# Performance work log

Hardware: AMD Instinct MI355X
Metric: run time of the kernel (lower is better)

## Reference

```python
import jax, jax.numpy as jnp
import numpy as np

IN_DIM = 128
OUT_DIM = 128
NUM_HEADS = 8
HEAD_DIM = OUT_DIM // NUM_HEADS  # 16
FFN_DIM = OUT_DIM * 2
LN_EPS = 1e-5


def _layer_norm(x, g, b):
    mu = jnp.mean(x, axis=-1, keepdims=True)
    var = jnp.var(x, axis=-1, keepdims=True)
    return (x - mu) * jax.lax.rsqrt(var + LN_EPS) * g + b


def setup_inputs() -> dict:
    key = jax.random.key(0)
    ks = jax.random.split(key, 12)
    B, N = 4, 2048
    s_in = 1.0 / np.sqrt(IN_DIM)
    s_out = 1.0 / np.sqrt(OUT_DIM)
    s_ffn = 1.0 / np.sqrt(FFN_DIM)
    return {
        "adj_matrix": jax.random.randint(ks[0], (N, N), 0, 2, dtype=jnp.int32),
        "h": jax.random.normal(ks[1], (B, N, IN_DIM), dtype=jnp.float32),
        # Q/K/V: Linear(in_dim, out_dim) with use_bias=False, stored as [in, out]
        "Wq": jax.random.uniform(ks[2], (IN_DIM, OUT_DIM), jnp.float32, -s_in, s_in),
        "Wk": jax.random.uniform(ks[3], (IN_DIM, OUT_DIM), jnp.float32, -s_in, s_in),
        "Wv": jax.random.uniform(ks[4], (IN_DIM, OUT_DIM), jnp.float32, -s_in, s_in),
        "Wo": jax.random.uniform(ks[5], (OUT_DIM, OUT_DIM), jnp.float32, -s_out, s_out),
        "bo": jnp.zeros((OUT_DIM,), jnp.float32),
        "ln1_g": jnp.ones((OUT_DIM,), jnp.float32),
        "ln1_b": jnp.zeros((OUT_DIM,), jnp.float32),
        "W1": jax.random.uniform(ks[6], (OUT_DIM, FFN_DIM), jnp.float32, -s_out, s_out),
        "b1": jnp.zeros((FFN_DIM,), jnp.float32),
        "W2": jax.random.uniform(ks[7], (FFN_DIM, OUT_DIM), jnp.float32, -s_ffn, s_ffn),
        "b2": jnp.zeros((OUT_DIM,), jnp.float32),
        "ln2_g": jnp.ones((OUT_DIM,), jnp.float32),
        "ln2_b": jnp.zeros((OUT_DIM,), jnp.float32),
    }


def reference(adj_matrix, h, Wq, Wk, Wv, Wo, bo, ln1_g, ln1_b,
              W1, b1, W2, b2, ln2_g, ln2_b):
    B, N, _ = h.shape
    # QKV projections -> [B, N, H, D]
    Q = (h @ Wq).reshape(B, N, NUM_HEADS, HEAD_DIM)
    K = (h @ Wk).reshape(B, N, NUM_HEADS, HEAD_DIM)
    V = (h @ Wv).reshape(B, N, NUM_HEADS, HEAD_DIM)
    scores = jnp.einsum('bnhd,bmhd->bhnm', Q, K) / jnp.sqrt(
        jnp.asarray(HEAD_DIM, jnp.float32))
    # adjacency-masked attention: mask broadcast over batch and heads
    mask = (adj_matrix == 0)[None, None, :, :]  # [1,1,N,N]
    scores = jnp.where(mask, -jnp.inf, scores)
    attn = jax.nn.softmax(scores, axis=-1)
    attn_out = jnp.einsum('bhnm,bmhd->bnhd', attn, V).reshape(B, N, OUT_DIM)
    # output projection + residual + LN
    x = h + (attn_out @ Wo + bo)
    x = _layer_norm(x, ln1_g, ln1_b)
    # FFN + residual + LN
    y = jax.nn.relu(x @ W1 + b1) @ W2 + b2
    x = _layer_norm(x + y, ln2_g, ln2_b)
    return x
```

## Files before the change

kernel.cpp:

```cpp
#include <hip/hip_runtime.h>

#define B_   4
#define N_   2048
#define DIM  128
#define NH   8
#define HD   16
#define FFN_ 256
#define LN_EPS 1e-5f
#define BN   (B_*N_)
#define LOG2E 1.44269504f

#if __has_builtin(__builtin_amdgcn_exp2f)
#define EXP2(x) __builtin_amdgcn_exp2f(x)
#else
#define EXP2(x) exp2f(x)
#endif

#if __has_builtin(__builtin_amdgcn_sbfe)
#define SBFE1(w, p) ((unsigned)__builtin_amdgcn_sbfe((int)(w), (p), 1))
#else
#define SBFE1(w, p) ((unsigned)(((int)((w) << (31 - (p)))) >> 31))
#endif

typedef __bf16 bf16x8 __attribute__((ext_vector_type(8)));
typedef short  s16x8  __attribute__((ext_vector_type(8)));
typedef float  f32x16 __attribute__((ext_vector_type(16)));
typedef unsigned int u32x4 __attribute__((ext_vector_type(4)));

template<class T> struct as_short_vec { using type = s16x8; };

template <class T>
__device__ auto mfma_try(T a, T b, f32x16 c, int)
    -> decltype(__builtin_amdgcn_mfma_f32_32x32x16_bf16(a, b, c, 0, 0, 0)) {
  return __builtin_amdgcn_mfma_f32_32x32x16_bf16(a, b, c, 0, 0, 0);
}
template <class T>
__device__ f32x16 mfma_try(T a, T b, f32x16 c, long) {
  return __builtin_amdgcn_mfma_f32_32x32x16_bf16(
      __builtin_bit_cast(typename as_short_vec<T>::type, a),
      __builtin_bit_cast(typename as_short_vec<T>::type, b), c, 0, 0, 0);
}
__device__ __forceinline__ f32x16 mfma_bf(bf16x8 a, bf16x8 b, f32x16 c) {
  return mfma_try(a, b, c, 0);
}

__global__ __launch_bounds__(256) void k_prep(
    const int* __restrict__ adj, const float* __restrict__ h,
    const float* __restrict__ W1, const float* __restrict__ W2,
    const float* __restrict__ Wq, const float* __restrict__ Wk,
    const float* __restrict__ Wv, const float* __restrict__ Wo,
    unsigned int* __restrict__ adjbT, __bf16* __restrict__ hb,
    __bf16* __restrict__ W1t, __bf16* __restrict__ W2t,
    __bf16* __restrict__ Wqt, __bf16* __restrict__ Wkt,
    __bf16* __restrict__ Wvt, __bf16* __restrict__ Wot) {
    const int blk = blockIdx.x;
    const int tid = threadIdx.x;
    if (blk < 16384) {
        long long idx = (long long)blk * 256 + tid;
        int v = adj[idx] != 0;
        unsigned long long m = __ballot(v);
        if ((tid & 63) == 0) {
            int q  = (int)(idx >> 11);
            int kc = ((int)idx & 2047) >> 5;
            adjbT[(size_t)kc * 2048 + q]       = (unsigned)m;
            adjbT[(size_t)(kc + 1) * 2048 + q] = (unsigned)(m >> 32);
        }
    } else if (blk < 16896) {
        const int g = (blk - 16384) * 256 + tid;
        const float* src = h + (size_t)g * 8;
        float4 f0 = *(const float4*)src, f1 = *(const float4*)(src + 4);
        bf16x8 v;
        v[0] = (__bf16)f0.x; v[1] = (__bf16)f0.y; v[2] = (__bf16)f0.z; v[3] = (__bf16)f0.w;
        v[4] = (__bf16)f1.x; v[5] = (__bf16)f1.y; v[6] = (__bf16)f1.z; v[7] = (__bf16)f1.w;
        *(bf16x8*)(hb + (size_t)g * 8) = v;
    } else {
        const int g = (blk - 16896) * 256 + tid;
        {
            int k = g >> 8, n = g & 255;
            W1t[(size_t)n * 128 + k] = (__bf16)W1[(size_t)k * 256 + n];
        }
        {
            int k = g >> 7, n = g & 127;
            W2t[(size_t)n * 256 + k] = (__bf16)W2[(size_t)k * 128 + n];
        }
        if (g < 16384) {
            int k = g >> 7, n = g & 127;
            size_t s = (size_t)k * 128 + n, d = (size_t)n * 128 + k;
            Wqt[d] = (__bf16)(Wq[s] * (0.25f * LOG2E));
            Wkt[d] = (__bf16)Wk[s];
            Wvt[d] = (__bf16)Wv[s];
            Wot[d] = (__bf16)Wo[s];
        }
    }
}

__global__ __launch_bounds__(256) void k_qkv(
    const __bf16* __restrict__ hb,
    const __bf16* __restrict__ Wqt, const __bf16* __restrict__ Wkt,
    const __bf16* __restrict__ Wvt,
    __bf16* __restrict__ Qb, __bf16* __restrict__ Kb, __bf16* __restrict__ Vt) {
    const int r0   = blockIdx.x * 32;
    const int tid  = threadIdx.x;
    const int w    = tid >> 6;
    const int lane = tid & 63;
    const int l31  = lane & 31, hi = lane >> 5;

    __shared__ __bf16 Hs[32 * 128];

    for (int i = tid; i < 512; i += 256) {
        int row = i >> 4, u = i & 15;
        bf16x8 v = *(const bf16x8*)(hb + (size_t)(r0 + row) * DIM + u * 8);
        int byte = (row * 256 + u * 16) ^ ((row & 7) << 4);
        *(bf16x8*)((char*)Hs + byte) = v;
    }
    __syncthreads();

    f32x16 aq, ak, av;
    #pragma unroll
    for (int i = 0; i < 16; ++i) { aq[i] = 0.f; ak[i] = 0.f; av[i] = 0.f; }
    #pragma unroll
    for (int kk = 0; kk < 8; ++kk) {
        int byte = (l31 * 256 + kk * 32 + hi * 16) ^ ((l31 & 7) << 4);
        bf16x8 a = *(const bf16x8*)((const char*)Hs + byte);
        const size_t wo = (size_t)(w * 32 + l31) * 128 + kk * 16 + hi * 8;
        aq = mfma_bf(a, *(const bf16x8*)(Wqt + wo), aq);
        ak = mfma_bf(a, *(const bf16x8*)(Wkt + wo), ak);
        av = mfma_bf(a, *(const bf16x8*)(Wvt + wo), av);
    }
    const int n  = w * 32 + l31;
    const int hh = n >> 4, d = n & 15;
    const int b  = r0 >> 11;
    const size_t qbase = (size_t)(b * NH + hh) * N_;
    const size_t vbase = ((size_t)(b * NH + hh) * HD + d) * N_;
    #pragma unroll
    for (int r = 0; r < 16; ++r) {
        int mm   = (r & 3) + 8 * (r >> 2) + 4 * hi;
        int nloc = (r0 & (N_ - 1)) + mm;
        size_t qk = (qbase + nloc) * HD + d;
        Qb[qk] = (__bf16)aq[r];
        Kb[qk] = (__bf16)ak[r];
        int gg = (nloc >> 2) & 7;
        int ng = (gg & 4) | ((gg & 1) << 1) | ((gg >> 1) & 1);
        Vt[vbase + ((nloc & ~31) | (ng << 2) | (nloc & 3))] = (__bf16)av[r];
    }
}

__global__ __launch_bounds__(512, 4) void k_attn(
    const __bf16* __restrict__ Qb, const __bf16* __restrict__ Kb,
    const __bf16* __restrict__ Vt, const unsigned int* __restrict__ adjbT,
    __bf16* __restrict__ AOb) {
    const int bid  = (blockIdx.x & 7) * 256 + (blockIdx.x >> 3);
    const int qt   = bid & 63;
    const int hh   = (bid >> 6) & 7;
    const int b    = bid >> 9;
    const int kq   = threadIdx.x >> 6;
    const int lane = threadIdx.x & 63;
    const int l31  = lane & 31, hi = lane >> 5;
    const int q     = qt * 32 + l31;
    const int kbase = kq * 256;
    const int NT    = 8;

    __shared__ float accL[7][64][9];

    const __bf16* Qh = Qb + (size_t)(b * NH + hh) * N_ * HD;
    const __bf16* Kh = Kb + (size_t)(b * NH + hh) * N_ * HD;
    const __bf16* Vh = Vt + ((size_t)(b * NH + hh) * HD + (l31 & 15)) * N_;
    const unsigned int* wp = adjbT + (size_t)(kq * NT) * 2048 + q;
    const bool vload = (l31 < 16);
    const bf16x8 ones8 = __builtin_bit_cast(bf16x8,
        u32x4{0x3F803F80u, 0x3F803F80u, 0x3F803F80u, 0x3F803F80u});

    bf16x8 qf = *(const bf16x8*)(Qh + (size_t)q * HD + hi * 8);

    f32x16 acc;
    #pragma unroll
    for (int i = 0; i < 16; ++i) acc[i] = 0.f;
    const f32x16 z = {};

    bf16x8 kf  = *(const bf16x8*)(Kh + (size_t)(kbase + l31) * HD + hi * 8);
    bf16x8 vfa = vload ? *(const bf16x8*)(Vh + kbase + hi * 8)      : ones8;
    bf16x8 vfb = vload ? *(const bf16x8*)(Vh + kbase + 16 + hi * 8) : ones8;
    unsigned int w32 = wp[0];

    for (int t = 0; t < NT; ++t) {
        const int tn = (t + 1 < NT) ? t + 1 : t;
        const int k1 = kbase + tn * 32;
        bf16x8 kf_n = *(const bf16x8*)(Kh + (size_t)(k1 + l31) * HD + hi * 8);
        bf16x8 vfa_n = vload ? *(const bf16x8*)(Vh + k1 + hi * 8)      : ones8;
        bf16x8 vfb_n = vload ? *(const bf16x8*)(Vh + k1 + 16 + hi * 8) : ones8;
        unsigned int w32_n = wp[(size_t)tn * 2048];

        f32x16 st = mfma_bf(kf, qf, z);

        float p[16];
        #pragma unroll
        for (int r = 0; r < 16; ++r) p[r] = EXP2(st[r]);
        bf16x8 pa, pb;
        #pragma unroll
        for (int r = 0; r < 8; ++r) { pa[r] = (__bf16)p[r]; pb[r] = (__bf16)p[r + 8]; }

        {
            const unsigned ws = w32 >> (4 * hi);
            u32x4 mA, mB;
            #pragma unroll
            for (int j = 0; j < 4; ++j) {
                const int pj = ((2 * j) & 3) + 8 * ((2 * j) >> 2);
                mA[j] = (SBFE1(ws, pj)      & 0xFFFFu) | (SBFE1(ws, pj + 1)  & 0xFFFF0000u);
                mB[j] = (SBFE1(ws, pj + 16) & 0xFFFFu) | (SBFE1(ws, pj + 17) & 0xFFFF0000u);
            }
            pa = __builtin_bit_cast(bf16x8, __builtin_bit_cast(u32x4, pa) & mA);
            pb = __builtin_bit_cast(bf16x8, __builtin_bit_cast(u32x4, pb) & mB);
        }

        acc = mfma_bf(vfa, pa, acc);
        acc = mfma_bf(vfb, pb, acc);

        kf = kf_n; vfa = vfa_n; vfb = vfb_n; w32 = w32_n;
    }

    if (kq != 0) {
        #pragma unroll
        for (int r = 0; r < 9; ++r) accL[kq - 1][lane][r] = acc[r];
    }
    __syncthreads();
    if (kq == 0) {
        float tot[9];
        #pragma unroll
        for (int r = 0; r < 9; ++r) {
            float v = acc[r];
            #pragma unroll
            for (int i = 0; i < 7; ++i) v += accL[i][lane][r];
            tot[r] = v;
        }
        float inv = 1.f / tot[8];
        bf16x8 ov;
        #pragma unroll
        for (int r = 0; r < 8; ++r) ov[r] = (__bf16)(tot[r] * inv);
        u32x4 ou = __builtin_bit_cast(u32x4, ov);
        __bf16* op = AOb + ((size_t)(b * N_ + q)) * DIM + hh * HD + 4 * hi;
        uint2 w0 = { ou[0], ou[1] }, w1 = { ou[2], ou[3] };
        *(uint2*)op       = w0;
        *(uint2*)(op + 8) = w1;
    }
}

__global__ __launch_bounds__(256) void k_proj_ln(
    const __bf16* __restrict__ AOb, const float* __restrict__ h,
    const __bf16* __restrict__ Wot, const float* __restrict__ bo,
    const float* __restrict__ g, const float* __restrict__ bln,
    __bf16* __restrict__ Xb) {
    const int r0   = blockIdx.x * 32;
    const int tid  = threadIdx.x;
    const int w    = tid >> 6;
    const int lane = tid & 63;
    const int l31  = lane & 31, hi = lane >> 5;

    __shared__ __bf16 As[32 * 128];
    __shared__ float  vv[32][DIM];

    for (int i = tid; i < 512; i += 256) {
        int row = i >> 4, u = i & 15;
        bf16x8 v = *(const bf16x8*)(AOb + (size_t)(r0 + row) * DIM + u * 8);
        int byte = (row * 256 + u * 16) ^ ((row & 7) << 4);
        *(bf16x8*)((char*)As + byte) = v;
    }
    __syncthreads();

    f32x16 acc;
    #pragma unroll
    for (int i = 0; i < 16; ++i) acc[i] = 0.f;
    #pragma unroll
    for (int kk = 0; kk < 8; ++kk) {
        int byte = (l31 * 256 + kk * 32 + hi * 16) ^ ((l31 & 7) << 4);
        bf16x8 a = *(const bf16x8*)((const char*)As + byte);
        acc = mfma_bf(a, *(const bf16x8*)(Wot + (size_t)(w * 32 + l31) * 128 + kk * 16 + hi * 8), acc);
    }
    {
        int n = w * 32 + l31;
        float bb = bo[n];
        #pragma unroll
        for (int r = 0; r < 16; ++r) {
            int mm = (r & 3) + 8 * (r >> 2) + 4 * hi;
            vv[mm][n] = acc[r] + bb + h[(size_t)(r0 + mm) * DIM + n];
        }
    }
    __syncthreads();

    const int ln = lane;
    float gc0 = g[ln], bc0 = bln[ln], gc1 = g[ln + 64], bc1 = bln[ln + 64];
    #pragma unroll
    for (int i = 0; i < 8; ++i) {
        int rr = w * 8 + i;
        float x0 = vv[rr][ln], x1 = vv[rr][ln + 64];
        float s = x0 + x1, s2 = x0 * x0 + x1 * x1;
        for (int off = 1; off < 64; off <<= 1) {
            s  += __shfl_xor(s,  off);
            s2 += __shfl_xor(s2, off);
        }
        float mu  = s * (1.f / DIM);
        float var = s2 * (1.f / DIM) - mu * mu;
        float rs  = rsqrtf(var + LN_EPS);
        size_t o = (size_t)(r0 + rr) * DIM;
        Xb[o + ln]      = (__bf16)((x0 - mu) * rs * gc0 + bc0);
        Xb[o + ln + 64] = (__bf16)((x1 - mu) * rs * gc1 + bc1);
    }
}

__global__ __launch_bounds__(256) void k_ffn_ln(
    const __bf16* __restrict__ Xb,
    const __bf16* __restrict__ W1t, const float* __restrict__ b1,
    const __bf16* __restrict__ W2t, const float* __restrict__ b2,
    const float* __restrict__ g, const float* __restrict__ bln,
    float* __restrict__ out) {
    const int r0   = blockIdx.x * 32;
    const int tid  = threadIdx.x;
    const int w    = tid >> 6;
    const int lane = tid & 63;
    const int l31  = lane & 31, hi = lane >> 5;

    __shared__ __bf16 Xs[32 * 128];
    __shared__ __bf16 Ts[32 * 256];
    __shared__ float  vv[32][DIM];

    for (int i = tid; i < 512; i += 256) {
        int row = i >> 4, u = i & 15;
        bf16x8 v = *(const bf16x8*)(Xb + (size_t)(r0 + row) * DIM + u * 8);
        int byte = (row * 256 + u * 16) ^ ((row & 7) << 4);
        *(bf16x8*)((char*)Xs + byte) = v;
    }
    __syncthreads();

    f32x16 acc1a, acc1b;
    #pragma unroll
    for (int i = 0; i < 16; ++i) { acc1a[i] = 0.f; acc1b[i] = 0.f; }
    #pragma unroll
    for (int kk = 0; kk < 8; ++kk) {
        int byte = (l31 * 256 + kk * 32 + hi * 16) ^ ((l31 & 7) << 4);
        bf16x8 a = *(const bf16x8*)((const char*)Xs + byte);
        bf16x8 bA = *(const bf16x8*)(W1t + (size_t)(w * 32 + l31) * 128 + kk * 16 + hi * 8);
        bf16x8 bB = *(const bf16x8*)(W1t + (size_t)((w + 4) * 32 + l31) * 128 + kk * 16 + hi * 8);
        acc1a = mfma_bf(a, bA, acc1a);
        acc1b = mfma_bf(a, bB, acc1b);
    }
    #pragma unroll
    for (int ct = 0; ct < 2; ++ct) {
        const f32x16& ac = ct ? acc1b : acc1a;
        int n = (w + ct * 4) * 32 + l31;
        float bb = b1[n];
        #pragma unroll
        for (int r = 0; r < 16; ++r) {
            int mm = (r & 3) + 8 * (r >> 2) + 4 * hi;
            float v = fmaxf(ac[r] + bb, 0.f);
            int byte = (mm * 512 + n * 2) ^ ((mm & 7) << 4);
            *(__bf16*)((char*)Ts + byte) = (__bf16)v;
        }
    }
    __syncthreads();

    f32x16 acc2;
    #pragma unroll
    for (int i = 0; i < 16; ++i) acc2[i] = 0.f;
    #pragma unroll
    for (int kk = 0; kk < 16; ++kk) {
        int byte = (l31 * 512 + kk * 32 + hi * 16) ^ ((l31 & 7) << 4);
        bf16x8 a = *(const bf16x8*)((const char*)Ts + byte);
        bf16x8 bb = *(const bf16x8*)(W2t + (size_t)(w * 32 + l31) * 256 + kk * 16 + hi * 8);
        acc2 = mfma_bf(a, bb, acc2);
    }
    {
        int n = w * 32 + l31;
        float bb = b2[n];
        #pragma unroll
        for (int r = 0; r < 16; ++r) {
            int mm = (r & 3) + 8 * (r >> 2) + 4 * hi;
            int byteR = (mm * 256 + n * 2) ^ ((mm & 7) << 4);
            float resid = (float)*(const __bf16*)((const char*)Xs + byteR);
            vv[mm][n] = acc2[r] + bb + resid;
        }
    }
    __syncthreads();

    const int ln = lane;
    float gc0 = g[ln], bc0 = bln[ln], gc1 = g[ln + 64], bc1 = bln[ln + 64];
    #pragma unroll
    for (int i = 0; i < 8; ++i) {
        int rr = w * 8 + i;
        float x0 = vv[rr][ln], x1 = vv[rr][ln + 64];
        float s = x0 + x1, s2 = x0 * x0 + x1 * x1;
        for (int off = 1; off < 64; off <<= 1) {
            s  += __shfl_xor(s,  off);
            s2 += __shfl_xor(s2, off);
        }
        float mu  = s * (1.f / DIM);
        float var = s2 * (1.f / DIM) - mu * mu;
        float rs  = rsqrtf(var + LN_EPS);
        size_t o = (size_t)(r0 + rr) * DIM;
        out[o + ln]      = (x0 - mu) * rs * gc0 + bc0;
        out[o + ln + 64] = (x1 - mu) * rs * gc1 + bc1;
    }
}

extern "C" void kernel_launch(void* const* d_in, const int* in_sizes, int n_in,
                              void* d_out, int out_size, void* d_ws, size_t ws_size,
                              hipStream_t stream) {
    const int*   adj = (const int*)  d_in[0];
    const float* h   = (const float*)d_in[1];
    const float* Wq  = (const float*)d_in[2];
    const float* Wk  = (const float*)d_in[3];
    const float* Wv  = (const float*)d_in[4];
    const float* Wo  = (const float*)d_in[5];
    const float* bo  = (const float*)d_in[6];
    const float* g1  = (const float*)d_in[7];
    const float* b1l = (const float*)d_in[8];
    const float* W1  = (const float*)d_in[9];
    const float* b1  = (const float*)d_in[10];
    const float* W2  = (const float*)d_in[11];
    const float* b2  = (const float*)d_in[12];
    const float* g2  = (const float*)d_in[13];
    const float* b2l = (const float*)d_in[14];
    float* out = (float*)d_out;

    __bf16* AOb = (__bf16*)d_ws;
    unsigned int* adjbT = (unsigned int*)(AOb + (size_t)BN * DIM);
    __bf16* Qb  = (__bf16*)(adjbT + (size_t)64 * 2048);
    __bf16* Kb  = Qb + (size_t)BN * DIM;
    __bf16* Vt  = Kb + (size_t)BN * DIM;
    __bf16* Xb  = Vt + (size_t)BN * DIM;
    __bf16* hb  = Xb + (size_t)BN * DIM;
    __bf16* W1t = hb + (size_t)BN * DIM;
    __bf16* W2t = W1t + (size_t)DIM * FFN_;
    __bf16* Wqt = W2t + (size_t)DIM * FFN_;
    __bf16* Wkt = Wqt + (size_t)DIM * DIM;
    __bf16* Wvt = Wkt + (size_t)DIM * DIM;
    __bf16* Wot = Wvt + (size_t)DIM * DIM;

    hipLaunchKernelGGL(k_prep, dim3(16384 + 512 + 128), dim3(256), 0, stream,
                       adj, h, W1, W2, Wq, Wk, Wv, Wo,
                       adjbT, hb, W1t, W2t, Wqt, Wkt, Wvt, Wot);
    hipLaunchKernelGGL(k_qkv, dim3(BN / 32), dim3(256), 0, stream,
                       hb, Wqt, Wkt, Wvt, Qb, Kb, Vt);
    hipLaunchKernelGGL(k_attn, dim3(B_ * NH * (N_ / 32)), dim3(512), 0, stream,
                       Qb, Kb, Vt, adjbT, AOb);
    hipLaunchKernelGGL(k_proj_ln, dim3(BN / 32), dim3(256), 0, stream,
                       AOb, h, Wot, bo, g1, b1l, Xb);
    hipLaunchKernelGGL(k_ffn_ln, dim3(BN / 32), dim3(256), 0, stream,
                       Xb, W1t, b1, W2t, b2, g2, b2l, out);
}
```

Measured before the change: 65.82 us.

## Fuse h conversion into QKV, merge proj/FFN kernels, use LUT for mask expansion

Converts h from float to bf16 directly inside the QKV kernel instead of a separate prep pass, removing the hb buffer round trip. Merges the output-projection+LN1 kernel with the FFN+LN2 kernel so the normalized activations stay in shared memory rather than going through global Xb, saving one launch. In attention, replaces per-bit sign-extract mask construction with a 16-entry shared-memory lookup table of uint2 masks. The fused tail kernel uses more shared memory per block, which may lower occupancy.

```diff
diff --git a/kernel.cpp b/kernel.cpp
--- a/kernel.cpp
+++ b/kernel.cpp
@@ -16,12 +16,6 @@
 #define EXP2(x) exp2f(x)
 #endif
 
-#if __has_builtin(__builtin_amdgcn_sbfe)
-#define SBFE1(w, p) ((unsigned)__builtin_amdgcn_sbfe((int)(w), (p), 1))
-#else
-#define SBFE1(w, p) ((unsigned)(((int)((w) << (31 - (p)))) >> 31))
-#endif
-
 typedef __bf16 bf16x8 __attribute__((ext_vector_type(8)));
 typedef short  s16x8  __attribute__((ext_vector_type(8)));
 typedef float  f32x16 __attribute__((ext_vector_type(16)));
@@ -45,11 +39,11 @@
 }
 
 __global__ __launch_bounds__(256) void k_prep(
-    const int* __restrict__ adj, const float* __restrict__ h,
+    const int* __restrict__ adj,
     const float* __restrict__ W1, const float* __restrict__ W2,
     const float* __restrict__ Wq, const float* __restrict__ Wk,
     const float* __restrict__ Wv, const float* __restrict__ Wo,
-    unsigned int* __restrict__ adjbT, __bf16* __restrict__ hb,
+    unsigned int* __restrict__ adjbT,
     __bf16* __restrict__ W1t, __bf16* __restrict__ W2t,
     __bf16* __restrict__ Wqt, __bf16* __restrict__ Wkt,
     __bf16* __restrict__ Wvt, __bf16* __restrict__ Wot) {
@@ -65,16 +59,8 @@
             adjbT[(size_t)kc * 2048 + q]       = (unsigned)m;
             adjbT[(size_t)(kc + 1) * 2048 + q] = (unsigned)(m >> 32);
         }
-    } else if (blk < 16896) {
+    } else {
         const int g = (blk - 16384) * 256 + tid;
-        const float* src = h + (size_t)g * 8;
-        float4 f0 = *(const float4*)src, f1 = *(const float4*)(src + 4);
-        bf16x8 v;
-        v[0] = (__bf16)f0.x; v[1] = (__bf16)f0.y; v[2] = (__bf16)f0.z; v[3] = (__bf16)f0.w;
-        v[4] = (__bf16)f1.x; v[5] = (__bf16)f1.y; v[6] = (__bf16)f1.z; v[7] = (__bf16)f1.w;
-        *(bf16x8*)(hb + (size_t)g * 8) = v;
-    } else {
-        const int g = (blk - 16896) * 256 + tid;
         {
             int k = g >> 8, n = g & 255;
             W1t[(size_t)n * 128 + k] = (__bf16)W1[(size_t)k * 256 + n];
@@ -95,7 +81,7 @@
 }
 
 __global__ __launch_bounds__(256) void k_qkv(
-    const __bf16* __restrict__ hb,
+    const float* __restrict__ h,
     const __bf16* __restrict__ Wqt, const __bf16* __restrict__ Wkt,
     const __bf16* __restrict__ Wvt,
     __bf16* __restrict__ Qb, __bf16* __restrict__ Kb, __bf16* __restrict__ Vt) {
@@ -109,7 +95,11 @@
 
     for (int i = tid; i < 512; i += 256) {
         int row = i >> 4, u = i & 15;
-        bf16x8 v = *(const bf16x8*)(hb + (size_t)(r0 + row) * DIM + u * 8);
+        const float* src = h + (size_t)(r0 + row) * DIM + u * 8;
+        float4 f0 = *(const float4*)src, f1 = *(const float4*)(src + 4);
+        bf16x8 v;
+        v[0] = (__bf16)f0.x; v[1] = (__bf16)f0.y; v[2] = (__bf16)f0.z; v[3] = (__bf16)f0.w;
+        v[4] = (__bf16)f1.x; v[5] = (__bf16)f1.y; v[6] = (__bf16)f1.z; v[7] = (__bf16)f1.w;
         int byte = (row * 256 + u * 16) ^ ((row & 7) << 4);
         *(bf16x8*)((char*)Hs + byte) = v;
     }
@@ -161,6 +151,14 @@
     const int NT    = 8;
 
     __shared__ float accL[7][64][9];
+    __shared__ uint2 lutM[16];
+
+    if (threadIdx.x < 16) {
+        unsigned v = threadIdx.x;
+        lutM[v].x = ((v & 1u) ? 0xFFFFu : 0u) | ((v & 2u) ? 0xFFFF0000u : 0u);
+        lutM[v].y = ((v & 4u) ? 0xFFFFu : 0u) | ((v & 8u) ? 0xFFFF0000u : 0u);
+    }
+    __syncthreads();
 
     const __bf16* Qh = Qb + (size_t)(b * NH + hh) * N_ * HD;
     const __bf16* Kh = Kb + (size_t)(b * NH + hh) * N_ * HD;
@@ -183,6 +181,12 @@
     unsigned int w32 = wp[0];
 
     for (int t = 0; t < NT; ++t) {
+        const unsigned ws = w32 >> (4 * hi);
+        uint2 e0 = lutM[ws & 15u];
+        uint2 e1 = lutM[(ws >> 8) & 15u];
+        uint2 e2 = lutM[(ws >> 16) & 15u];
+        uint2 e3 = lutM[(ws >> 24) & 15u];
+
         const int tn = (t + 1 < NT) ? t + 1 : t;
         const int k1 = kbase + tn * 32;
         bf16x8 kf_n = *(const bf16x8*)(Kh + (size_t)(k1 + l31) * HD + hi * 8);
@@ -199,18 +203,10 @@
         #pragma unroll
         for (int r = 0; r < 8; ++r) { pa[r] = (__bf16)p[r]; pb[r] = (__bf16)p[r + 8]; }
 
-        {
-            const unsigned ws = w32 >> (4 * hi);
-            u32x4 mA, mB;
-            #pragma unroll
-            for (int j = 0; j < 4; ++j) {
-                const int pj = ((2 * j) & 3) + 8 * ((2 * j) >> 2);
-                mA[j] = (SBFE1(ws, pj)      & 0xFFFFu) | (SBFE1(ws, pj + 1)  & 0xFFFF0000u);
-                mB[j] = (SBFE1(ws, pj + 16) & 0xFFFFu) | (SBFE1(ws, pj + 17) & 0xFFFF0000u);
-            }
-            pa = __builtin_bit_cast(bf16x8, __builtin_bit_cast(u32x4, pa) & mA);
-            pb = __builtin_bit_cast(bf16x8, __builtin_bit_cast(u32x4, pb) & mB);
-        }
+        u32x4 mA = {e0.x, e0.y, e1.x, e1.y};
+        u32x4 mB = {e2.x, e2.y, e3.x, e3.y};
+        pa = __builtin_bit_cast(bf16x8, __builtin_bit_cast(u32x4, pa) & mA);
+        pb = __builtin_bit_cast(bf16x8, __builtin_bit_cast(u32x4, pb) & mB);
 
         acc = mfma_bf(vfa, pa, acc);
         acc = mfma_bf(vfb, pb, acc);
@@ -244,73 +240,13 @@
     }
 }
 
-__global__ __launch_bounds__(256) void k_proj_ln(
+__global__ __launch_bounds__(256) void k_tail(
     const __bf16* __restrict__ AOb, const float* __restrict__ h,
     const __bf16* __restrict__ Wot, const float* __restrict__ bo,
-    const float* __restrict__ g, const float* __restrict__ bln,
-    __bf16* __restrict__ Xb) {
-    const int r0   = blockIdx.x * 32;
-    const int tid  = threadIdx.x;
-    const int w    = tid >> 6;
-    const int lane = tid & 63;
-    const int l31  = lane & 31, hi = lane >> 5;
-
-    __shared__ __bf16 As[32 * 128];
-    __shared__ float  vv[32][DIM];
-
-    for (int i = tid; i < 512; i += 256) {
-        int row = i >> 4, u = i & 15;
-        bf16x8 v = *(const bf16x8*)(AOb + (size_t)(r0 + row) * DIM + u * 8);
-        int byte = (row * 256 + u * 16) ^ ((row & 7) << 4);
-        *(bf16x8*)((char*)As + byte) = v;
-    }
-    __syncthreads();
-
-    f32x16 acc;
-    #pragma unroll
-    for (int i = 0; i < 16; ++i) acc[i] = 0.f;
-    #pragma unroll
-    for (int kk = 0; kk < 8; ++kk) {
-        int byte = (l31 * 256 + kk * 32 + hi * 16) ^ ((l31 & 7) << 4);
-        bf16x8 a = *(const bf16x8*)((const char*)As + byte);
-        acc = mfma_bf(a, *(const bf16x8*)(Wot + (size_t)(w * 32 + l31) * 128 + kk * 16 + hi * 8), acc);
-    }
-    {
-        int n = w * 32 + l31;
-        float bb = bo[n];
-        #pragma unroll
-        for (int r = 0; r < 16; ++r) {
-            int mm = (r & 3) + 8 * (r >> 2) + 4 * hi;
-            vv[mm][n] = acc[r] + bb + h[(size_t)(r0 + mm) * DIM + n];
-        }
-    }
-    __syncthreads();
-
-    const int ln = lane;
-    float gc0 = g[ln], bc0 = bln[ln], gc1 = g[ln + 64], bc1 = bln[ln + 64];
-    #pragma unroll
-    for (int i = 0; i < 8; ++i) {
-        int rr = w * 8 + i;
-        float x0 = vv[rr][ln], x1 = vv[rr][ln + 64];
-        float s = x0 + x1, s2 = x0 * x0 + x1 * x1;
-        for (int off = 1; off < 64; off <<= 1) {
-            s  += __shfl_xor(s,  off);
-            s2 += __shfl_xor(s2, off);
-        }
-        float mu  = s * (1.f / DIM);
-        float var = s2 * (1.f / DIM) - mu * mu;
-        float rs  = rsqrtf(var + LN_EPS);
-        size_t o = (size_t)(r0 + rr) * DIM;
-        Xb[o + ln]      = (__bf16)((x0 - mu) * rs * gc0 + bc0);
-        Xb[o + ln + 64] = (__bf16)((x1 - mu) * rs * gc1 + bc1);
-    }
-}
-
-__global__ __launch_bounds__(256) void k_ffn_ln(
-    const __bf16* __restrict__ Xb,
+    const float* __restrict__ g1, const float* __restrict__ b1ln,
     const __bf16* __restrict__ W1t, const float* __restrict__ b1,
     const __bf16* __restrict__ W2t, const float* __restrict__ b2,
-    const float* __restrict__ g, const float* __restrict__ bln,
+    const float* __restrict__ g2, const float* __restrict__ b2ln,
     float* __restrict__ out) {
     const int r0   = blockIdx.x * 32;
     const int tid  = threadIdx.x;
@@ -318,15 +254,59 @@
     const int lane = tid & 63;
     const int l31  = lane & 31, hi = lane >> 5;
 
+    __shared__ __bf16 As[32 * 128];
     __shared__ __bf16 Xs[32 * 128];
     __shared__ __bf16 Ts[32 * 256];
     __shared__ float  vv[32][DIM];
 
     for (int i = tid; i < 512; i += 256) {
         int row = i >> 4, u = i & 15;
-        bf16x8 v = *(const bf16x8*)(Xb + (size_t)(r0 + row) * DIM + u * 8);
+        bf16x8 v = *(const bf16x8*)(AOb + (size_t)(r0 + row) * DIM + u * 8);
         int byte = (row * 256 + u * 16) ^ ((row & 7) << 4);
-        *(bf16x8*)((char*)Xs + byte) = v;
+        *(bf16x8*)((char*)As + byte) = v;
+    }
+    __syncthreads();
+
+    f32x16 acc;
+    #pragma unroll
+    for (int i = 0; i < 16; ++i) acc[i] = 0.f;
+    #pragma unroll
+    for (int kk = 0; kk < 8; ++kk) {
+        int byte = (l31 * 256 + kk * 32 + hi * 16) ^ ((l31 & 7) << 4);
+        bf16x8 a = *(const bf16x8*)((const char*)As + byte);
+        acc = mfma_bf(a, *(const bf16x8*)(Wot + (size_t)(w * 32 + l31) * 128 + kk * 16 + hi * 8), acc);
+    }
+    {
+        int n = w * 32 + l31;
+        float bb = bo[n];
+        #pragma unroll
+        for (int r = 0; r < 16; ++r) {
+            int mm = (r & 3) + 8 * (r >> 2) + 4 * hi;
+            vv[mm][n] = acc[r] + bb + h[(size_t)(r0 + mm) * DIM + n];
+        }
+    }
+    __syncthreads();
+
+    {
+        const int ln = lane;
+        float gc0 = g1[ln], bc0 = b1ln[ln], gc1 = g1[ln + 64], bc1 = b1ln[ln + 64];
+        #pragma unroll
+        for (int i = 0; i < 8; ++i) {
+            int rr = w * 8 + i;
+            float x0 = vv[rr][ln], x1 = vv[rr][ln + 64];
+            float s = x0 + x1, s2 = x0 * x0 + x1 * x1;
+            for (int off = 1; off < 64; off <<= 1) {
+                s  += __shfl_xor(s,  off);
+                s2 += __shfl_xor(s2, off);
+            }
+            float mu  = s * (1.f / DIM);
+            float var = s2 * (1.f / DIM) - mu * mu;
+            float rs  = rsqrtf(var + LN_EPS);
+            int byte0 = (rr * 256 + ln * 2) ^ ((rr & 7) << 4);
+            int byte1 = (rr * 256 + (ln + 64) * 2) ^ ((rr & 7) << 4);
+            *(__bf16*)((char*)Xs + byte0) = (__bf16)((x0 - mu) * rs * gc0 + bc0);
+            *(__bf16*)((char*)Xs + byte1) = (__bf16)((x1 - mu) * rs * gc1 + bc1);
+        }
     }
     __syncthreads();
 
@@ -380,23 +360,25 @@
     }
     __syncthreads();
 
-    const int ln = lane;
-    float gc0 = g[ln], bc0 = bln[ln], gc1 = g[ln + 64], bc1 = bln[ln + 64];
-    #pragma unroll
-    for (int i = 0; i < 8; ++i) {
-        int rr = w * 8 + i;
-        float x0 = vv[rr][ln], x1 = vv[rr][ln + 64];
-        float s = x0 + x1, s2 = x0 * x0 + x1 * x1;
-        for (int off = 1; off < 64; off <<= 1) {
-            s  += __shfl_xor(s,  off);
-            s2 += __shfl_xor(s2, off);
-        }
-        float mu  = s * (1.f / DIM);
-        float var = s2 * (1.f / DIM) - mu * mu;
-        float rs  = rsqrtf(var + LN_EPS);
-        size_t o = (size_t)(r0 + rr) * DIM;
-        out[o + ln]      = (x0 - mu) * rs * gc0 + bc0;
-        out[o + ln + 64] = (x1 - mu) * rs * gc1 + bc1;
+    {
+        const int ln = lane;
+        float gc0 = g2[ln], bc0 = b2ln[ln], gc1 = g2[ln + 64], bc1 = b2ln[ln + 64];
+        #pragma unroll
+        for (int i = 0; i < 8; ++i) {
+            int rr = w * 8 + i;
+            float x0 = vv[rr][ln], x1 = vv[rr][ln + 64];
+            float s = x0 + x1, s2 = x0 * x0 + x1 * x1;
+            for (int off = 1; off < 64; off <<= 1) {
+                s  += __shfl_xor(s,  off);
+                s2 += __shfl_xor(s2, off);
+            }
+            float mu  = s * (1.f / DIM);
+            float var = s2 * (1.f / DIM) - mu * mu;
+            float rs  = rsqrtf(var + LN_EPS);
+            size_t o = (size_t)(r0 + rr) * DIM;
+            out[o + ln]      = (x0 - mu) * rs * gc0 + bc0;
+            out[o + ln + 64] = (x1 - mu) * rs * gc1 + bc1;
+        }
     }
 }
 
@@ -425,24 +407,20 @@
     __bf16* Qb  = (__bf16*)(adjbT + (size_t)64 * 2048);
     __bf16* Kb  = Qb + (size_t)BN * DIM;
     __bf16* Vt  = Kb + (size_t)BN * DIM;
-    __bf16* Xb  = Vt + (size_t)BN * DIM;
-    __bf16* hb  = Xb + (size_t)BN * DIM;
-    __bf16* W1t = hb + (size_t)BN * DIM;
+    __bf16* W1t = Vt + (size_t)BN * DIM;
     __bf16* W2t = W1t + (size_t)DIM * FFN_;
     __bf16* Wqt = W2t + (size_t)DIM * FFN_;
     __bf16* Wkt = Wqt + (size_t)DIM * DIM;
     __bf16* Wvt = Wkt + (size_t)DIM * DIM;
     __bf16* Wot = Wvt + (size_t)DIM * DIM;
 
-    hipLaunchKernelGGL(k_prep, dim3(16384 + 512 + 128), dim3(256), 0, stream,
-                       adj, h, W1, W2, Wq, Wk, Wv, Wo,
-                       adjbT, hb, W1t, W2t, Wqt, Wkt, Wvt, Wot);
+    hipLaunchKernelGGL(k_prep, dim3(16384 + 128), dim3(256), 0, stream,
+                       adj, W1, W2, Wq, Wk, Wv, Wo,
+                       adjbT, W1t, W2t, Wqt, Wkt, Wvt, Wot);
     hipLaunchKernelGGL(k_qkv, dim3(BN / 32), dim3(256), 0, stream,
-                       hb, Wqt, Wkt, Wvt, Qb, Kb, Vt);
+                       h, Wqt, Wkt, Wvt, Qb, Kb, Vt);
     hipLaunchKernelGGL(k_attn, dim3(B_ * NH * (N_ / 32)), dim3(512), 0, stream,
                        Qb, Kb, Vt, adjbT, AOb);
-    hipLaunchKernelGGL(k_proj_ln, dim3(BN / 32), dim3(256), 0, stream,
-                       AOb, h, Wot, bo, g1, b1l, Xb);
-    hipLaunchKernelGGL(k_ffn_ln, dim3(BN / 32), dim3(256), 0, stream,
-                       Xb, W1t, b1, W2t, b2, g2, b2l, out);
-}
+    hipLaunchKernelGGL(k_tail, dim3(BN / 32), dim3(256), 0, stream,
+                       AOb, h, Wot, bo, g1, b1l, W1t, b1, W2t, b2, g2, b2l, out);
+}
```

After: 63.38 us. -3.7%, faster.
